# Kernel optimization log

Measured on AMD Instinct MI355X. Metric: run time of the kernel, lower is better.

Reference implementation:

```python
import jax, jax.numpy as jnp
import numpy as np

N, E, D_IN, D_OUT, R = 50000, 800000, 128, 128, 8


def setup_inputs() -> dict:
    key = jax.random.key(0)
    ks = jax.random.split(key, 6)
    x = jax.random.normal(ks[0], (N, D_IN), dtype=jnp.float32)
    W_rel = jax.random.normal(ks[1], (R, D_IN, D_OUT), dtype=jnp.float32) * (1.0 / np.sqrt(D_IN))
    W_self_w = jax.random.normal(ks[2], (D_OUT, D_IN), dtype=jnp.float32) * (1.0 / np.sqrt(D_IN))
    W_self_b = jax.random.normal(ks[3], (D_OUT,), dtype=jnp.float32) * 0.01
    edge_index = jax.random.randint(ks[4], (2, E), 0, N, dtype=jnp.int32)
    edge_type = jax.random.randint(ks[5], (E,), 0, R, dtype=jnp.int32)
    return {"x": x, "W_rel": W_rel, "W_self_w": W_self_w, "W_self_b": W_self_b,
            "edge_index": edge_index, "edge_type": edge_type}


def reference(x, W_rel, W_self_w, W_self_b, edge_index, edge_type):
    n = x.shape[0]
    # self-loop linear (nn.Linear: y = x @ W.T + b)
    out = x @ W_self_w.T + W_self_b
    src = edge_index[0]
    dst = edge_index[1]
    # Per-relation transform of all nodes: h[r, n, :] = x[n] @ W_rel[r]
    # (mathematically identical to per-edge bmm(x[src], W_rel[rel]))
    h = jnp.einsum('nd,rdo->rno', x, W_rel)  # [R, N, D_OUT]
    msg = h[edge_type, src]                   # [E, D_OUT] gather
    agg = jax.ops.segment_sum(msg, dst, num_segments=n)  # scatter-add
    deg = jax.ops.segment_sum(jnp.ones_like(dst, dtype=x.dtype), dst, num_segments=n)
    deg = jnp.maximum(deg, 1.0)[:, None]
    out = jax.nn.relu(out + agg / deg)
    # dropout p=0.0 / eval mode -> identity
    return out
```

## Files before the change

### kernel.cpp

```cpp
#include <hip/hip_runtime.h>
#include <hip/hip_bf16.h>


#define D 128
#define RNUM 8
#define KREL (RNUM * D)
#define KTOT (KREL + D)
#define ZCH 64
#define ZNB 64
#define ZSP 72

#define BSHIFT 6
#define BRANGE 64
#define BCAP   2048
#define NBKT_MAX 784
#define CSTRIDE 16

typedef short short8 __attribute__((ext_vector_type(8)));
typedef float float4v __attribute__((ext_vector_type(4)));
typedef float float2v __attribute__((ext_vector_type(2)));

static __device__ __forceinline__ unsigned int f2b(float f) {
    unsigned int u = __float_as_uint(f);
    return (u + 0x7fffu + ((u >> 16) & 1u)) >> 16;
}
static __device__ __forceinline__ float b2f_lo(unsigned int u) {
    return __uint_as_float(u << 16);
}
static __device__ __forceinline__ float b2f_hi(unsigned int u) {
    return __uint_as_float(u & 0xffff0000u);
}

static __device__ __forceinline__ void gl_lds16(const void* g, void* l) {
    __builtin_amdgcn_global_load_lds(
        (const __attribute__((address_space(1))) unsigned int*)g,
        (__attribute__((address_space(3))) unsigned int*)l, 16, 0, 0);
}

__global__ __launch_bounds__(256) void prep_coarse_kernel(
        const float* __restrict__ x,
        const float* __restrict__ W_rel,
        const float* __restrict__ W_self,
        const int* __restrict__ ei, const int* __restrict__ et,
        unsigned short* __restrict__ xb,
        unsigned short* __restrict__ Wcol,
        int* __restrict__ gcur, int* __restrict__ data,
        int Nn, int E, int xb_blocks, int wc_blocks, int nbkt) {
    __shared__ int cnt[NBKT_MAX];
    if (blockIdx.x < (unsigned)xb_blocks) {
        int t = blockIdx.x * 256 + threadIdx.x;
        int n = t >> 5;
        int c = (t & 31) * 4;
        if (n >= Nn) return;
        float4 v = *(const float4*)(x + (size_t)n * D + c);
        unsigned int p0 = f2b(v.x) | (f2b(v.y) << 16);
        unsigned int p1 = f2b(v.z) | (f2b(v.w) << 16);
        *(uint2*)(xb + (size_t)n * D + c) = make_uint2(p0, p1);
    } else if (blockIdx.x < (unsigned)(xb_blocks + wc_blocks)) {
        int idx = (blockIdx.x - xb_blocks) * 256 + threadIdx.x;
        if (idx >= KTOT * D) return;
        int c = idx >> 7;
        int k = idx & 127;
        float v = (c < KREL)
            ? W_rel[(size_t)((c >> 7) * D + k) * D + (c & 127)]
            : W_self[(size_t)(c - KREL) * D + k];
        Wcol[idx] = (unsigned short)f2b(v);
    } else {
        int blk = blockIdx.x - xb_blocks - wc_blocks;
        int t = threadIdx.x;
        for (int i = t; i < nbkt; i += 256) cnt[i] = 0;
        __syncthreads();

        int rec[8], rb[8], rk[8];
        int e0 = blk * 2048;
#pragma unroll
        for (int j = 0; j < 8; ++j) {
            int e = e0 + j * 256 + t;
            bool ok = e < E;
            int s = ok ? ei[e] : 0;
            int d = ok ? ei[E + e] : 0;
            int r = ok ? et[e] : 0;
            int bkt = d >> BSHIFT;
            rec[j] = s | ((d & (BRANGE - 1)) << 16) | (r << 22);
            rb[j] = ok ? bkt : -1;
            rk[j] = ok ? atomicAdd(&cnt[bkt], 1) : 0;
        }
        __syncthreads();

        for (int i = t; i < nbkt; i += 256) {
            int c = cnt[i];
            if (c) cnt[i] = i * BCAP + atomicAdd(&gcur[i * CSTRIDE], c);
        }
        __syncthreads();

#pragma unroll
        for (int j = 0; j < 8; ++j) {
            if (rb[j] >= 0) {
                int pos = cnt[rb[j]] + rk[j];
                if (pos < (rb[j] + 1) * BCAP)
                    data[pos] = rec[j];
            }
        }
    }
}

__global__ __launch_bounds__(256) void zgemm_fine_kernel(
        const unsigned short* __restrict__ xb,
        const unsigned short* __restrict__ Wcol,
        unsigned short* __restrict__ Z,
        int* __restrict__ data, const int* __restrict__ gcur,
        int* __restrict__ offsets, int* __restrict__ deg,
        int Nn, int nstrip, int spx, int zg) {
    __shared__ __align__(16) char smem[25600];

    if ((int)blockIdx.x < zg) {
        unsigned short* Ws = (unsigned short*)smem;
        unsigned short* Zs = (unsigned short*)(smem + 16384);

        const int xcd = blockIdx.x & 7;
        const int i0  = blockIdx.x >> 3;
        const int strip = xcd * spx + i0 / 18;
        const int chunk = i0 % 18;
        if (strip >= nstrip) return;

        const int tid  = threadIdx.x;
        const int lane = tid & 63;
        const int w    = tid >> 6;
        const int l16  = lane & 15;
        const int q    = lane >> 4;
        const int c0   = chunk * ZCH;
        const int n0   = strip * ZNB;
        const int n    = n0 + w * 16 + l16;

        short8 xq[4];
#pragma unroll
        for (int kw = 0; kw < 4; ++kw)
            xq[kw] = *(const short8*)(xb + (size_t)n * D + kw * 32 + q * 8);

#pragma unroll
        for (int i = 0; i < 4; ++i) {
            int s = i * 256 + w * 64 + lane;
            int c = s >> 4;
            int p = (s & 15) ^ (c & 15);
            gl_lds16(Wcol + (size_t)(c0 + c) * D + p * 8,
                     &Ws[(size_t)(i * 256 + w * 64) * 8]);
        }
        __syncthreads();

        float4v acc[4] = {};
#pragma unroll
        for (int cg = 0; cg < 4; ++cg) {
#pragma unroll
            for (int kw = 0; kw < 4; ++kw) {
                short8 a = *(const short8*)(
                    &Ws[(((cg * 16 + l16) << 4) + ((kw * 4 + q) ^ l16)) * 8]);
                acc[cg] = __builtin_amdgcn_mfma_f32_16x16x32_bf16(
                    a, xq[kw], acc[cg], 0, 0, 0);
            }
        }

#pragma unroll
        for (int cg = 0; cg < 4; ++cg) {
            unsigned int lo = f2b(acc[cg][0]) | (f2b(acc[cg][1]) << 16);
            unsigned int hi = f2b(acc[cg][2]) | (f2b(acc[cg][3]) << 16);
            *(uint2*)(&Zs[(w * 16 + l16) * ZSP + cg * 16 + q * 4]) = make_uint2(lo, hi);
        }
        __syncthreads();

        {
            int row = tid >> 2;
            int pc  = (tid & 3) * 8;
            short8 z0 = *(const short8*)(&Zs[row * ZSP + pc]);
            short8 z1 = *(const short8*)(&Zs[row * ZSP + pc + 32]);
            unsigned short* dst = Z + (size_t)(n0 + row) * KTOT + c0;
            *(short8*)(dst + pc)      = z0;
            *(short8*)(dst + pc + 32) = z1;
        }
    } else {
        int* recs = (int*)smem;
        int* hist = (int*)(smem + 8192);
        int b = blockIdx.x - zg;
        int t = threadIdx.x;
        int gbase = b * BCAP;
        int cnt = gcur[b * CSTRIDE];
        if (cnt > BCAP) cnt = BCAP;

        for (int i = t; i < BRANGE * RNUM; i += 256) hist[i] = 0;
        __syncthreads();

        for (int i = t; i < cnt; i += 256) {
            int rec = data[gbase + i];
            recs[i] = rec;
            int n = (rec >> 16) & (BRANGE - 1);
            int r = (rec >> 22) & 7;
            atomicAdd(&hist[n * RNUM + r], 1);
        }
        __syncthreads();

        if (t < BRANGE) {
            int dsum = 0;
#pragma unroll
            for (int r = 0; r < RNUM; ++r) dsum += hist[t * RNUM + r];
            int pad = (dsum + 7) & ~7;
            int x = pad;
            for (int off = 1; off < 64; off <<= 1) {
                int y = __shfl_up(x, off);
                if (t >= off) x += y;
            }
            int nb = gbase + (x - pad);
            int n0 = b * BRANGE + t;
            if (n0 < Nn) { offsets[n0] = nb; deg[n0] = dsum; }
            for (int i = dsum; i < pad; ++i)
                data[nb + i] = (int)0xF0000000u;
            int q = nb;
#pragma unroll
            for (int r = 0; r < RNUM; ++r) {
                int c = hist[t * RNUM + r]; hist[t * RNUM + r] = q; q += c;
            }
        }
        __syncthreads();

        for (int i = t; i < cnt; i += 256) {
            int rec = recs[i];
            int n = (rec >> 16) & (BRANGE - 1);
            int r = (rec >> 22) & 7;
            int pos = atomicAdd(&hist[n * RNUM + r], 1);
            data[pos] = (rec & 0xFFFF) | (r << 28);
        }
    }
}

__global__ __launch_bounds__(256) void gather_kernel(
        const unsigned short* __restrict__ Z,
        const int* __restrict__ offsets,
        const int* __restrict__ deg,
        const int* __restrict__ sorted,
        const float* __restrict__ bias,
        float* __restrict__ out,
        int Nn) {
    int node = blockIdx.x * 4 + (threadIdx.x >> 6);
    if (node >= Nn) return;
    int lane = threadIdx.x & 63;
    int laneoff = lane * 2;

    int b0 = __builtin_amdgcn_readfirstlane(offsets[node]);
    int dg = __builtin_amdgcn_readfirstlane(deg[node]);
    float inv = 1.0f / fmaxf((float)dg, 1.0f);
    int bulk = dg & ~7;
    int rem  = dg & 7;

    float2v racc = {0.0f, 0.0f};

    for (int e = b0; e < b0 + bulk; e += 8) {
        int pv[8];
#pragma unroll
        for (int j = 0; j < 8; ++j)
            pv[j] = __builtin_amdgcn_readfirstlane(sorted[e + j]);
        unsigned int u[8];
#pragma unroll
        for (int j = 0; j < 8; ++j) {
            int src = pv[j] & 0xFFFF;
            int rel = (((unsigned)pv[j]) >> 28) & 7;
            u[j] = *(const unsigned int*)(Z + (size_t)src * KTOT + rel * D + laneoff);
        }
#pragma unroll
        for (int j = 0; j < 8; ++j) {
            racc.x += b2f_lo(u[j]);
            racc.y += b2f_hi(u[j]);
        }
    }
    if (rem) {
        int e = b0 + bulk;
        int pv[8];
#pragma unroll
        for (int j = 0; j < 8; ++j)
            pv[j] = __builtin_amdgcn_readfirstlane(sorted[e + j]);
        unsigned int u[8];
#pragma unroll
        for (int j = 0; j < 8; ++j) {
            int src = pv[j] & 0xFFFF;
            int rel = (((unsigned)pv[j]) >> 28) & 7;
            u[j] = *(const unsigned int*)(Z + (size_t)src * KTOT + rel * D + laneoff);
        }
#pragma unroll
        for (int j = 0; j < 8; ++j) {
            if (j < rem) {
                racc.x += b2f_lo(u[j]);
                racc.y += b2f_hi(u[j]);
            }
        }
    }

    unsigned int zs = *(const unsigned int*)(Z + (size_t)node * KTOT + KREL + laneoff);
    float bx = bias[laneoff];
    float by = bias[laneoff + 1];
    float o0 = fmaxf(b2f_lo(zs) + bx + racc.x * inv, 0.0f);
    float o1 = fmaxf(b2f_hi(zs) + by + racc.y * inv, 0.0f);
    *(float2*)(out + (size_t)node * D + laneoff) = make_float2(o0, o1);
}

extern "C" void kernel_launch(void* const* d_in, const int* in_sizes, int n_in,
                              void* d_out, int out_size, void* d_ws, size_t ws_size,
                              hipStream_t stream) {
    const float* x      = (const float*)d_in[0];
    const float* W_rel  = (const float*)d_in[1];
    const float* W_self = (const float*)d_in[2];
    const float* W_bias = (const float*)d_in[3];
    const int*   ei     = (const int*)d_in[4];
    const int*   et     = (const int*)d_in[5];

    const int Nn = in_sizes[0] / D;
    const int E  = in_sizes[4] / 2;
    const int npad = ((Nn + ZNB - 1) / ZNB) * ZNB;
    const int nstrip = npad / ZNB;
    const int spx  = (nstrip + 7) / 8;
    const int zg   = spx * 8 * 18;
    const int nbkt = (Nn + BRANGE - 1) >> BSHIFT;
    const int gz   = nbkt * CSTRIDE;

    char* p = (char*)d_ws;
    auto take = [&](size_t bytes) { char* q = p; p += (bytes + 255) & ~(size_t)255; return q; };
    unsigned short* Z    = (unsigned short*)take((size_t)npad * KTOT * sizeof(unsigned short));
    unsigned short* xb   = (unsigned short*)take((size_t)npad * D * sizeof(unsigned short));
    unsigned short* Wcol = (unsigned short*)take((size_t)KTOT * D * sizeof(unsigned short));
    int* offsets = (int*)take((size_t)Nn * sizeof(int));
    int* deg     = (int*)take((size_t)Nn * sizeof(int));
    int* gcur    = (int*)take((size_t)gz * sizeof(int));
    int* data    = (int*)take((size_t)nbkt * BCAP * sizeof(int));

    const int xb_blocks = (Nn * 32 + 255) / 256;
    const int wc_blocks = (KTOT * D + 255) / 256;
    const int co_blocks = (E + 2047) / 2048;

    hipMemsetAsync(gcur, 0, (size_t)gz * sizeof(int), stream);
    prep_coarse_kernel<<<xb_blocks + wc_blocks + co_blocks, 256, 0, stream>>>(
        x, W_rel, W_self, ei, et, xb, Wcol, gcur, data, Nn, E,
        xb_blocks, wc_blocks, nbkt);
    zgemm_fine_kernel<<<zg + nbkt, 256, 0, stream>>>(
        xb, Wcol, Z, data, gcur, offsets, deg, Nn, nstrip, spx, zg);
    gather_kernel<<<(Nn + 3) / 4, 256, 0, stream>>>(Z, offsets, deg, data, W_bias,
                                                    (float*)d_out, Nn);
}
```

Before: 194.6 us.

## Replace atomic bucket scatter with per-block local sort and count matrix

Edge bucketing no longer takes global atomics on per-bucket cursors. Each coarse block now sorts its 2048 edges by destination bucket in LDS, writes them contiguously, and records per-bucket offsets in a count matrix. Fine blocks walk that matrix to collect their edges and no longer sub-sort by relation. Records now store a precomputed Z element offset, padding entries point at a zeroed dummy Z row, and the gather loop is unrolled to 16 loads. In exchange, each fine block must scan up to nco segments serially per thread, and it loses relation locality in the gather.

Measured after the change: 186.5 us. 1.04x faster.

```diff
diff --git a/kernel.cpp b/kernel.cpp
--- a/kernel.cpp
+++ b/kernel.cpp
@@ -13,12 +13,10 @@
 #define BSHIFT 6
 #define BRANGE 64
 #define BCAP   2048
-#define NBKT_MAX 784
-#define CSTRIDE 16
+#define CROW   784
 
 typedef short short8 __attribute__((ext_vector_type(8)));
 typedef float float4v __attribute__((ext_vector_type(4)));
-typedef float float2v __attribute__((ext_vector_type(2)));
 
 static __device__ __forceinline__ unsigned int f2b(float f) {
     unsigned int u = __float_as_uint(f);
@@ -44,20 +42,26 @@
         const int* __restrict__ ei, const int* __restrict__ et,
         unsigned short* __restrict__ xb,
         unsigned short* __restrict__ Wcol,
-        int* __restrict__ gcur, int* __restrict__ data,
-        int Nn, int E, int xb_blocks, int wc_blocks, int nbkt) {
-    __shared__ int cnt[NBKT_MAX];
+        int* __restrict__ data,
+        int* __restrict__ cmat,
+        unsigned short* __restrict__ zrow,
+        int Nn, int E, int xb_blocks, int wc_blocks, int co_blocks) {
+    __shared__ int cnt[CROW];
+    __shared__ int ps[256];
+    __shared__ int recs[2048];
+    const int t = threadIdx.x;
+
     if (blockIdx.x < (unsigned)xb_blocks) {
-        int t = blockIdx.x * 256 + threadIdx.x;
-        int n = t >> 5;
-        int c = (t & 31) * 4;
+        int tt = blockIdx.x * 256 + t;
+        int n = tt >> 5;
+        int c = (tt & 31) * 4;
         if (n >= Nn) return;
         float4 v = *(const float4*)(x + (size_t)n * D + c);
         unsigned int p0 = f2b(v.x) | (f2b(v.y) << 16);
         unsigned int p1 = f2b(v.z) | (f2b(v.w) << 16);
         *(uint2*)(xb + (size_t)n * D + c) = make_uint2(p0, p1);
     } else if (blockIdx.x < (unsigned)(xb_blocks + wc_blocks)) {
-        int idx = (blockIdx.x - xb_blocks) * 256 + threadIdx.x;
+        int idx = (blockIdx.x - xb_blocks) * 256 + t;
         if (idx >= KTOT * D) return;
         int c = idx >> 7;
         int k = idx & 127;
@@ -65,10 +69,9 @@
             ? W_rel[(size_t)((c >> 7) * D + k) * D + (c & 127)]
             : W_self[(size_t)(c - KREL) * D + k];
         Wcol[idx] = (unsigned short)f2b(v);
-    } else {
+    } else if (blockIdx.x < (unsigned)(xb_blocks + wc_blocks + co_blocks)) {
         int blk = blockIdx.x - xb_blocks - wc_blocks;
-        int t = threadIdx.x;
-        for (int i = t; i < nbkt; i += 256) cnt[i] = 0;
+        for (int i = t; i < CROW; i += 256) cnt[i] = 0;
         __syncthreads();
 
         int rec[8], rb[8], rk[8];
@@ -80,27 +83,51 @@
             int s = ok ? ei[e] : 0;
             int d = ok ? ei[E + e] : 0;
             int r = ok ? et[e] : 0;
-            int bkt = d >> BSHIFT;
-            rec[j] = s | ((d & (BRANGE - 1)) << 16) | (r << 22);
-            rb[j] = ok ? bkt : -1;
-            rk[j] = ok ? atomicAdd(&cnt[bkt], 1) : 0;
-        }
-        __syncthreads();
-
-        for (int i = t; i < nbkt; i += 256) {
-            int c = cnt[i];
-            if (c) cnt[i] = i * BCAP + atomicAdd(&gcur[i * CSTRIDE], c);
-        }
-        __syncthreads();
-
-#pragma unroll
-        for (int j = 0; j < 8; ++j) {
-            if (rb[j] >= 0) {
-                int pos = cnt[rb[j]] + rk[j];
-                if (pos < (rb[j] + 1) * BCAP)
-                    data[pos] = rec[j];
+            rec[j] = (s * KTOT + r * D) | ((d & (BRANGE - 1)) << 26);
+            rb[j] = ok ? (d >> BSHIFT) : -1;
+            rk[j] = ok ? atomicAdd(&cnt[d >> BSHIFT], 1) : 0;
+        }
+        __syncthreads();
+
+        int s4 = 0;
+#pragma unroll
+        for (int i = 0; i < 4; ++i) {
+            int idx = t * 4 + i;
+            if (idx < CROW) s4 += cnt[idx];
+        }
+        ps[t] = s4;
+        __syncthreads();
+        for (int off = 1; off < 256; off <<= 1) {
+            int v = (t >= off) ? ps[t - off] : 0;
+            __syncthreads();
+            ps[t] += v;
+            __syncthreads();
+        }
+        int ex = t ? ps[t - 1] : 0;
+#pragma unroll
+        for (int i = 0; i < 4; ++i) {
+            int idx = t * 4 + i;
+            if (idx < CROW) {
+                int c = cnt[idx];
+                cnt[idx] = ex;
+                cmat[(size_t)blk * CROW + idx] = ex;
+                ex += c;
             }
         }
+        __syncthreads();
+
+#pragma unroll
+        for (int j = 0; j < 8; ++j)
+            if (rb[j] >= 0) recs[cnt[rb[j]] + rk[j]] = rec[j];
+        __syncthreads();
+
+        int4* dsrc = (int4*)recs;
+        int4* ddst = (int4*)(data + (size_t)blk * 2048);
+        ddst[t * 2]     = dsrc[t * 2];
+        ddst[t * 2 + 1] = dsrc[t * 2 + 1];
+    } else {
+        for (int i = t; i < KTOT / 4; i += 256)
+            ((uint2*)zrow)[i] = make_uint2(0u, 0u);
     }
 }
 
@@ -108,9 +135,11 @@
         const unsigned short* __restrict__ xb,
         const unsigned short* __restrict__ Wcol,
         unsigned short* __restrict__ Z,
-        int* __restrict__ data, const int* __restrict__ gcur,
+        const int* __restrict__ data,
+        const int* __restrict__ cmat,
+        int* __restrict__ sorted,
         int* __restrict__ offsets, int* __restrict__ deg,
-        int Nn, int nstrip, int spx, int zg) {
+        int Nn, int nstrip, int spx, int zg, int nco, int zoff) {
     __shared__ __align__(16) char smem[25600];
 
     if ((int)blockIdx.x < zg) {
@@ -177,56 +206,51 @@
             *(short8*)(dst + pc + 32) = z1;
         }
     } else {
-        int* recs = (int*)smem;
-        int* hist = (int*)(smem + 8192);
+        int* rs   = (int*)smem;
+        int* re   = (int*)(smem + 1568);
+        int* hist = (int*)(smem + 3136);
+        int* curp = (int*)(smem + 3392);
         int b = blockIdx.x - zg;
         int t = threadIdx.x;
-        int gbase = b * BCAP;
-        int cnt = gcur[b * CSTRIDE];
-        if (cnt > BCAP) cnt = BCAP;
-
-        for (int i = t; i < BRANGE * RNUM; i += 256) hist[i] = 0;
-        __syncthreads();
-
-        for (int i = t; i < cnt; i += 256) {
-            int rec = data[gbase + i];
-            recs[i] = rec;
-            int n = (rec >> 16) & (BRANGE - 1);
-            int r = (rec >> 22) & 7;
-            atomicAdd(&hist[n * RNUM + r], 1);
-        }
+
+        for (int i = t; i < BRANGE; i += 256) hist[i] = 0;
+        for (int i = t; i < nco; i += 256) {
+            int s = cmat[(size_t)i * CROW + b];
+            int e = cmat[(size_t)i * CROW + b + 1];
+            rs[i] = i * 2048 + s;
+            re[i] = i * 2048 + e;
+        }
+        __syncthreads();
+
+        for (int i = t; i < nco; i += 256)
+            for (int k = rs[i]; k < re[i]; ++k)
+                atomicAdd(&hist[((unsigned)data[k]) >> 26], 1);
         __syncthreads();
 
         if (t < BRANGE) {
-            int dsum = 0;
-#pragma unroll
-            for (int r = 0; r < RNUM; ++r) dsum += hist[t * RNUM + r];
+            int dsum = hist[t];
             int pad = (dsum + 7) & ~7;
             int x = pad;
             for (int off = 1; off < 64; off <<= 1) {
                 int y = __shfl_up(x, off);
                 if (t >= off) x += y;
             }
-            int nb = gbase + (x - pad);
+            int nb = b * BCAP + (x - pad);
             int n0 = b * BRANGE + t;
             if (n0 < Nn) { offsets[n0] = nb; deg[n0] = dsum; }
             for (int i = dsum; i < pad; ++i)
-                data[nb + i] = (int)0xF0000000u;
-            int q = nb;
-#pragma unroll
-            for (int r = 0; r < RNUM; ++r) {
-                int c = hist[t * RNUM + r]; hist[t * RNUM + r] = q; q += c;
+                sorted[nb + i] = zoff;
+            curp[t] = nb;
+        }
+        __syncthreads();
+
+        for (int i = t; i < nco; i += 256)
+            for (int k = rs[i]; k < re[i]; ++k) {
+                int rc = data[k];
+                int node = ((unsigned)rc) >> 26;
+                int pos = atomicAdd(&curp[node], 1);
+                sorted[pos] = rc & 0x03FFFFFF;
             }
-        }
-        __syncthreads();
-
-        for (int i = t; i < cnt; i += 256) {
-            int rec = recs[i];
-            int n = (rec >> 16) & (BRANGE - 1);
-            int r = (rec >> 22) & 7;
-            int pos = atomicAdd(&hist[n * RNUM + r], 1);
-            data[pos] = (rec & 0xFFFF) | (r << 28);
-        }
     }
 }
 
@@ -246,56 +270,47 @@
     int b0 = __builtin_amdgcn_readfirstlane(offsets[node]);
     int dg = __builtin_amdgcn_readfirstlane(deg[node]);
     float inv = 1.0f / fmaxf((float)dg, 1.0f);
-    int bulk = dg & ~7;
-    int rem  = dg & 7;
-
-    float2v racc = {0.0f, 0.0f};
-
-    for (int e = b0; e < b0 + bulk; e += 8) {
+    int len = (dg + 7) & ~7;
+
+    float racx = 0.0f, racy = 0.0f;
+    int e = b0;
+
+    for (; e + 16 <= b0 + len; e += 16) {
+        int pv[16];
+#pragma unroll
+        for (int j = 0; j < 16; ++j)
+            pv[j] = __builtin_amdgcn_readfirstlane(sorted[e + j]);
+        unsigned int u[16];
+#pragma unroll
+        for (int j = 0; j < 16; ++j)
+            u[j] = *(const unsigned int*)(Z + (size_t)pv[j] + laneoff);
+#pragma unroll
+        for (int j = 0; j < 16; ++j) {
+            racx += b2f_lo(u[j]);
+            racy += b2f_hi(u[j]);
+        }
+    }
+    if (e < b0 + len) {
         int pv[8];
 #pragma unroll
         for (int j = 0; j < 8; ++j)
             pv[j] = __builtin_amdgcn_readfirstlane(sorted[e + j]);
         unsigned int u[8];
 #pragma unroll
+        for (int j = 0; j < 8; ++j)
+            u[j] = *(const unsigned int*)(Z + (size_t)pv[j] + laneoff);
+#pragma unroll
         for (int j = 0; j < 8; ++j) {
-            int src = pv[j] & 0xFFFF;
-            int rel = (((unsigned)pv[j]) >> 28) & 7;
-            u[j] = *(const unsigned int*)(Z + (size_t)src * KTOT + rel * D + laneoff);
-        }
-#pragma unroll
-        for (int j = 0; j < 8; ++j) {
-            racc.x += b2f_lo(u[j]);
-            racc.y += b2f_hi(u[j]);
-        }
-    }
-    if (rem) {
-        int e = b0 + bulk;
-        int pv[8];
-#pragma unroll
-        for (int j = 0; j < 8; ++j)
-            pv[j] = __builtin_amdgcn_readfirstlane(sorted[e + j]);
-        unsigned int u[8];
-#pragma unroll
-        for (int j = 0; j < 8; ++j) {
-            int src = pv[j] & 0xFFFF;
-            int rel = (((unsigned)pv[j]) >> 28) & 7;
-            u[j] = *(const unsigned int*)(Z + (size_t)src * KTOT + rel * D + laneoff);
-        }
-#pragma unroll
-        for (int j = 0; j < 8; ++j) {
-            if (j < rem) {
-                racc.x += b2f_lo(u[j]);
-                racc.y += b2f_hi(u[j]);
-            }
+            racx += b2f_lo(u[j]);
+            racy += b2f_hi(u[j]);
         }
     }
 
     unsigned int zs = *(const unsigned int*)(Z + (size_t)node * KTOT + KREL + laneoff);
     float bx = bias[laneoff];
     float by = bias[laneoff + 1];
-    float o0 = fmaxf(b2f_lo(zs) + bx + racc.x * inv, 0.0f);
-    float o1 = fmaxf(b2f_hi(zs) + by + racc.y * inv, 0.0f);
+    float o0 = fmaxf(b2f_lo(zs) + bx + racx * inv, 0.0f);
+    float o1 = fmaxf(b2f_hi(zs) + by + racy * inv, 0.0f);
     *(float2*)(out + (size_t)node * D + laneoff) = make_float2(o0, o1);
 }
 
@@ -316,28 +331,30 @@
     const int spx  = (nstrip + 7) / 8;
     const int zg   = spx * 8 * 18;
     const int nbkt = (Nn + BRANGE - 1) >> BSHIFT;
-    const int gz   = nbkt * CSTRIDE;
+    const int nco  = (E + 2047) / 2048;
+    const int zoff = npad * KTOT;
 
     char* p = (char*)d_ws;
     auto take = [&](size_t bytes) { char* q = p; p += (bytes + 255) & ~(size_t)255; return q; };
-    unsigned short* Z    = (unsigned short*)take((size_t)npad * KTOT * sizeof(unsigned short));
+    unsigned short* Z    = (unsigned short*)take(((size_t)npad * KTOT + KTOT) * sizeof(unsigned short));
     unsigned short* xb   = (unsigned short*)take((size_t)npad * D * sizeof(unsigned short));
     unsigned short* Wcol = (unsigned short*)take((size_t)KTOT * D * sizeof(unsigned short));
     int* offsets = (int*)take((size_t)Nn * sizeof(int));
     int* deg     = (int*)take((size_t)Nn * sizeof(int));
-    int* gcur    = (int*)take((size_t)gz * sizeof(int));
-    int* data    = (int*)take((size_t)nbkt * BCAP * sizeof(int));
+    int* data    = (int*)take((size_t)nco * 2048 * sizeof(int));
+    int* cmat    = (int*)take((size_t)nco * CROW * sizeof(int));
+    int* sorted  = (int*)take((size_t)nbkt * BCAP * sizeof(int));
+    unsigned short* zrow = Z + (size_t)npad * KTOT;
 
     const int xb_blocks = (Nn * 32 + 255) / 256;
     const int wc_blocks = (KTOT * D + 255) / 256;
-    const int co_blocks = (E + 2047) / 2048;
-
-    hipMemsetAsync(gcur, 0, (size_t)gz * sizeof(int), stream);
-    prep_coarse_kernel<<<xb_blocks + wc_blocks + co_blocks, 256, 0, stream>>>(
-        x, W_rel, W_self, ei, et, xb, Wcol, gcur, data, Nn, E,
-        xb_blocks, wc_blocks, nbkt);
+
+    prep_coarse_kernel<<<xb_blocks + wc_blocks + nco + 1, 256, 0, stream>>>(
+        x, W_rel, W_self, ei, et, xb, Wcol, data, cmat, zrow,
+        Nn, E, xb_blocks, wc_blocks, nco);
     zgemm_fine_kernel<<<zg + nbkt, 256, 0, stream>>>(
-        xb, Wcol, Z, data, gcur, offsets, deg, Nn, nstrip, spx, zg);
-    gather_kernel<<<(Nn + 3) / 4, 256, 0, stream>>>(Z, offsets, deg, data, W_bias,
+        xb, Wcol, Z, data, cmat, sorted, offsets, deg,
+        Nn, nstrip, spx, zg, nco, zoff);
+    gather_kernel<<<(Nn + 3) / 4, 256, 0, stream>>>(Z, offsets, deg, sorted, W_bias,
                                                     (float*)d_out, Nn);
 }
```
